# Optimization experiments

Hardware: AMD Instinct MI355X
Metric: run time of the kernel (lower is better)

The kernel has to match this reference:

```python
import jax, jax.numpy as jnp
import numpy as np

N = 200_000      # active voxels
C_IN = 128
C_OUT = 128
GRID = 128
K = 27           # 3x3x3 submanifold kernel offsets
EPS = 1e-4       # scn BatchNormalization default eps
LEAK = 0.333     # scn LeakyReLU default leakiness


def _build_neighbor_idx(rng):
    # unique active voxel coords via unique linear keys in GRID^3
    keys = rng.choice(GRID ** 3, size=N, replace=False).astype(np.int64)
    z = keys % GRID
    y = (keys // GRID) % GRID
    x = keys // (GRID * GRID)
    coords = np.stack([x, y, z], axis=1)  # [N,3]
    order = np.argsort(keys)
    sorted_keys = keys[order]
    offs = np.array([(dx, dy, dz) for dx in (-1, 0, 1)
                     for dy in (-1, 0, 1) for dz in (-1, 0, 1)], dtype=np.int64)
    nb = np.full((N, K), -1, dtype=np.int32)
    for k in range(K):
        q = coords + offs[k]  # [N,3]
        inb = np.all((q >= 0) & (q < GRID), axis=1)
        qk = (q[:, 0] * GRID + q[:, 1]) * GRID + q[:, 2]
        pos = np.searchsorted(sorted_keys, qk)
        pos = np.clip(pos, 0, N - 1)
        hit = inb & (sorted_keys[pos] == qk)
        nb[:, k] = np.where(hit, order[pos].astype(np.int32), -1)
    return nb


def setup_inputs() -> dict:
    key = jax.random.key(0)
    k1, k2 = jax.random.split(key)
    rng = np.random.default_rng(0)
    neighbor_idx = jnp.asarray(_build_neighbor_idx(rng))       # [N,27] int32, -1 = inactive
    features = jax.random.normal(k1, (N, C_IN), dtype=jnp.float32)
    # per-offset conv weights, scn-style init scale
    W = jax.random.normal(k2, (K, C_IN, C_OUT), dtype=jnp.float32) * (1.0 / np.sqrt(K * C_IN))
    b = jnp.zeros((C_OUT,), dtype=jnp.float32)
    gamma = jnp.ones((C_OUT,), dtype=jnp.float32)
    beta = jnp.zeros((C_OUT,), dtype=jnp.float32)
    return {"features": features, "W": W, "b": b, "gamma": gamma,
            "beta": beta, "neighbor_idx": neighbor_idx}


def reference(features, W, b, gamma, beta, neighbor_idx):
    # Submanifold 3D conv: output only at active sites; gather active neighbors.
    valid = (neighbor_idx >= 0)                      # [N,27] bool
    idx = jnp.where(valid, neighbor_idx, 0)          # safe gather index
    out = jnp.broadcast_to(b, (features.shape[0], C_OUT))
    for k in range(K):  # fixed structural loop over 27 kernel offsets
        xk = features[idx[:, k]] * valid[:, k:k + 1].astype(features.dtype)  # [N,C_IN]
        out = out + xk @ W[k]                                                # [N,C_OUT]
    # BatchNormalization over all active sites (training-mode batch stats)
    mean = jnp.mean(out, axis=0)
    var = jnp.var(out, axis=0)
    out = (out - mean) * jax.lax.rsqrt(var + EPS) * gamma + beta
    # LeakyReLU (scn default leakiness 0.333)
    return jnp.where(out > 0, out, LEAK * out)
```

## Files before the change

### kernel.cpp

```cpp
#include <hip/hip_runtime.h>
#include <hip/hip_bf16.h>

#define N_VOX 200000
#define CI 128
#define CO 128
#define KK 27
#define BM 96
#define NBLK96 2084
#define NBLKFB 1563
#define NSTEP 54
#define LEAK 0.333f
#define BN_EPS 1e-4f
#define SENT 0x3FFFFu
#define ACC_STRIDE 132
#define RB_CAP 48
#define RB_PAD 1344

typedef unsigned short u16;
typedef unsigned int u32;
typedef __attribute__((ext_vector_type(8))) short short8;
typedef __attribute__((ext_vector_type(4))) float f32x4;

typedef const __attribute__((address_space(1))) u32* gptr_t;
typedef __attribute__((address_space(3))) u32* lptr_t;

__device__ __forceinline__ u16 f2bf(float f) {
  union { float f; u32 u; } x; x.f = f;
  return (u16)((x.u + 0x7FFFu + ((x.u >> 16) & 1u)) >> 16);
}
__device__ __forceinline__ float bf2f(u16 h) {
  union { u32 u; float f; } x; x.u = ((u32)h) << 16;
  return x.f;
}
__device__ __forceinline__ u16 cvt_bf(float f) {
  union { __hip_bfloat16 h; u16 u; } c;
  c.h = __float2bfloat16(f);
  return c.u;
}
__device__ __forceinline__ int kbase_of(int k) {
  return (k < 13) ? k * RB_CAP : (k == 13 ? 13 * RB_CAP : 13 * RB_CAP + BM + (k - 14) * RB_CAP);
}

__global__ __launch_bounds__(256) void fcast_kernel(const float* __restrict__ f,
                                                    u16* __restrict__ fb) {
  size_t i = ((size_t)blockIdx.x * 256 + threadIdx.x) * 8;
  float4 a = *(const float4*)(f + i);
  float4 b = *(const float4*)(f + i + 4);
  u16 t[8];
  t[0] = cvt_bf(a.x); t[1] = cvt_bf(a.y); t[2] = cvt_bf(a.z); t[3] = cvt_bf(a.w);
  t[4] = cvt_bf(b.x); t[5] = cvt_bf(b.y); t[6] = cvt_bf(b.z); t[7] = cvt_bf(b.w);
  *(uint4*)(fb + i) = *(const uint4*)t;
}

__global__ __launch_bounds__(256) void wcast3_kernel(const float* __restrict__ W,
                                                     u16* __restrict__ Wt3) {
  int gid = blockIdx.x * 256 + threadIdx.x;
  int lane = gid & 63, chunk = gid >> 6;
  int ks = chunk & 3, nf = (chunk >> 2) & 7, k = chunk >> 5;
  int lr = lane & 15, lg = lane >> 4;
  int co = nf * 16 + lr;
  int ci0 = ks * 32 + lg * 8;
  const float* Wk = W + (size_t)k * CI * CO;
  u16 t[8];
#pragma unroll
  for (int e = 0; e < 8; ++e) t[e] = f2bf(Wk[(ci0 + e) * CO + co]);
  *(uint4*)(Wt3 + (size_t)gid * 8) = *(const uint4*)t;
}

__global__ __launch_bounds__(256, 4) void conv_sp_kernel(
    const u16* __restrict__ featb, const u16* __restrict__ Wt3,
    const int* __restrict__ nb, const u16* __restrict__ zp,
    float* __restrict__ out, float* __restrict__ partial) {
  __shared__ __align__(16) char smem[31312];
  u16* const accb = (u16*)smem;
  u32* const rb_lds = (u32*)(smem + 25344);
  int* const cnt_lds = (int*)(smem + 30784);
  int* const wcnt = (int*)(smem + 30896);
  u32* const wl = (u32*)(smem + 30912);
  int* const wl_n = (int*)(smem + 31296);
  float* const ps = (float*)smem;

  const int tid = threadIdx.x;
  const int bid = blockIdx.x;
  const int row0 = bid * BM;
  const int lane = tid & 63;
  const int w = tid >> 6;

  for (int i = tid; i < (BM * ACC_STRIDE) / 2; i += 256) ((u32*)accb)[i] = 0u;
  if (tid < 16) rb_lds[RB_PAD + tid] = SENT;

  {
    const bool inrow = (tid < BM) && (row0 + tid < N_VOX);
    const int* nbp = nb + (size_t)(row0 + tid) * KK;
    int vv[KK];
#pragma unroll
    for (int k = 0; k < KK; ++k) vv[k] = (k != 13 && inrow) ? nbp[k] : -1;
    if (tid < BM)
      rb_lds[13 * RB_CAP + tid] = ((u32)tid << 18) | (inrow ? (u32)(row0 + tid) : SENT);
    if (tid == 0) cnt_lds[13] = BM;
#pragma unroll
    for (int k = 0; k < KK; ++k) {
      if (k == 13) continue;
      bool valid = vv[k] >= 0;
      unsigned long long m = __ballot(valid);
      if (lane == 0) wcnt[w] = (int)__popcll(m);
      __syncthreads();
      int pos = (int)__popcll(m & ((1ull << lane) - 1ull)) + (w == 1 ? wcnt[0] : 0);
      int cnt = wcnt[0] + wcnt[1]; if (cnt > RB_CAP) cnt = RB_CAP;
      int kb = kbase_of(k);
      if (valid && pos < RB_CAP) rb_lds[kb + pos] = ((u32)tid << 18) | (u32)vv[k];
      int pe = (cnt + 15) & ~15;
      for (int i = cnt + tid; i < pe; i += 256) rb_lds[kb + i] = SENT;
      if (tid == 0) cnt_lds[k] = cnt;
      __syncthreads();
    }
  }

  if (tid == 0) {
    int n = 0;
    for (int k = 0; k < KK; ++k) {
      int cnt = cnt_lds[k];
      int kb = kbase_of(k);
      int ntk = (cnt + 15) >> 4;
      for (int t = 0; t < ntk; ++t) wl[n++] = ((u32)k << 11) | (u32)(kb + t * 16);
    }
    if (n & 1) wl[n++] = (u32)RB_PAD;
    wl_n[0] = n;
  }
  __syncthreads();

  const int wv = w;
  const int lr = lane & 15, lg = lane >> 4;
  const int colbase = wv * 32 + lr;
  const int nt = wl_n[0];

  auto loadTile = [&](u32 d, uint4& sc, short8* a) {
    int off = (int)(d & 0x7FFu);
    u32 es = rb_lds[off + lr];
    sc = *(const uint4*)&rb_lds[off + lg * 4];
    u32 src = es & SENT;
    const u16* ap = (src == SENT) ? zp : (featb + (size_t)src * CI);
#pragma unroll
    for (int ks = 0; ks < 4; ++ks) a[ks] = *(const short8*)(ap + ks * 32 + lg * 8);
  };
  auto loadB = [&](u32 d, short8* b) {
    int k = (int)(d >> 11);
    const u16* wb = Wt3 + (size_t)(k * 32 + wv * 8) * 512 + lane * 8;
#pragma unroll
    for (int j = 0; j < 8; ++j) b[j] = *(const short8*)(wb + j * 512);
  };
  auto mfma_scat = [&](const short8* a, const short8* b, const uint4& sc) {
    f32x4 c0 = {0.f, 0.f, 0.f, 0.f}, c1 = {0.f, 0.f, 0.f, 0.f};
#pragma unroll
    for (int ks = 0; ks < 4; ++ks) {
      c0 = __builtin_amdgcn_mfma_f32_16x16x32_bf16(a[ks], b[ks], c0, 0, 0, 0);
      c1 = __builtin_amdgcn_mfma_f32_16x16x32_bf16(a[ks], b[4 + ks], c1, 0, 0, 0);
    }
    u32 e[4] = {sc.x, sc.y, sc.z, sc.w};
#pragma unroll
    for (int r = 0; r < 4; ++r) {
      if (e[r] != SENT) {
        int i0 = (int)(e[r] >> 18) * ACC_STRIDE + colbase;
        accb[i0] = f2bf(bf2f(accb[i0]) + c0[r]);
        accb[i0 + 16] = f2bf(bf2f(accb[i0 + 16]) + c1[r]);
      }
    }
  };

  for (int i = 0; i < nt; i += 2) {
    u32 d0 = wl[i], d1 = wl[i + 1];
    uint4 sc0, sc1;
    short8 a0[4], a1[4], b0[8], b1[8];
    loadTile(d0, sc0, a0);
    loadTile(d1, sc1, a1);
    loadB(d0, b0);
    __builtin_amdgcn_sched_barrier(0);
    mfma_scat(a0, b0, sc0);
    loadB(d1, b1);
    __builtin_amdgcn_sched_barrier(0);
    mfma_scat(a1, b1, sc1);
  }
  __syncthreads();

  float s4[4] = {0.f, 0.f, 0.f, 0.f}, q4[4] = {0.f, 0.f, 0.f, 0.f};
  const int col4 = (tid & 31) * 4;
  const int rgrp = tid >> 5;
#pragma unroll
  for (int i = 0; i < 12; ++i) {
    int row = rgrp + i * 8;
    const u16* ap = &accb[row * ACC_STRIDE + col4];
    float4 v;
    v.x = bf2f(ap[0]); v.y = bf2f(ap[1]); v.z = bf2f(ap[2]); v.w = bf2f(ap[3]);
    int grow = row0 + row;
    if (grow < N_VOX) {
      *(float4*)&out[(size_t)grow * CO + col4] = v;
      s4[0] += v.x; q4[0] += v.x * v.x;
      s4[1] += v.y; q4[1] += v.y * v.y;
      s4[2] += v.z; q4[2] += v.z * v.z;
      s4[3] += v.w; q4[3] += v.w * v.w;
    }
  }
  __syncthreads();
#pragma unroll
  for (int j = 0; j < 4; ++j) {
    ps[rgrp * 128 + col4 + j] = s4[j];
    ps[1024 + rgrp * 128 + col4 + j] = q4[j];
  }
  __syncthreads();
  {
    int col = tid & 127, which = tid >> 7;
    float acc = 0.f;
#pragma unroll
    for (int g = 0; g < 8; ++g) acc += ps[which * 1024 + g * 128 + col];
    partial[(size_t)bid * 256 + tid] = acc;
  }
}

__global__ __launch_bounds__(256, 2) void conv_fb_kernel(
    const float* __restrict__ feat, const u16* __restrict__ Wt3,
    const int* __restrict__ nb, float* __restrict__ out,
    float* __restrict__ partial) {
  __shared__ __align__(16) char smem[46592];
  u16* const Ab = (u16*)smem;
  int* const nbs = (int*)(smem + 32768);
  float* const sq = (float*)smem;

  const int tid = threadIdx.x;
  const int bid = blockIdx.x;
  const int row0 = bid * 128;

  for (int i = tid; i < 128 * KK; i += 256) {
    int gi = row0 * KK + i;
    nbs[i] = (gi < N_VOX * KK) ? nb[gi] : -1;
  }
  __syncthreads();

  const int lane = tid & 63;
  const int wv = tid >> 6;
  const int wr = wv >> 1, wc = wv & 1;
  const int lr = lane & 15, lg = lane >> 4;
  const int arow = tid >> 1;
  const int acol = (tid & 1) * 32;

  f32x4 acc[4][4];
#pragma unroll
  for (int m = 0; m < 4; ++m)
#pragma unroll
    for (int n = 0; n < 4; ++n) acc[m][n] = (f32x4){0.f, 0.f, 0.f, 0.f};

  float4 af[8];
  short8 b0[8], b1[8];

  auto issueAf = [&](int s) {
    int k = s >> 1, half = (s & 1) * 64;
    int src = nbs[arow * KK + k];
    if (src >= 0) {
      const float4* p = (const float4*)(feat + (size_t)src * CI + half + acol);
#pragma unroll
      for (int j = 0; j < 8; ++j) af[j] = p[j];
    } else {
#pragma unroll
      for (int j = 0; j < 8; ++j) af[j] = (float4){0.f, 0.f, 0.f, 0.f};
    }
  };
  auto loadB = [&](int s, short8* bn) {
    int k = s >> 1, half = s & 1;
#pragma unroll
    for (int n = 0; n < 4; ++n)
#pragma unroll
      for (int ks = 0; ks < 2; ++ks)
        bn[n * 2 + ks] = *(const short8*)(Wt3 +
            (size_t)((k * 32 + (wc * 4 + n) * 4) + half * 2 + ks) * 512 + lane * 8);
  };
  auto writeA = [&](u16* Adst) {
    int v = arow & 7;
#pragma unroll
    for (int q = 0; q < 4; ++q) {
      u16 t8[8];
#pragma unroll
      for (int i = 0; i < 2; ++i) {
        float4 f = af[q * 2 + i];
        t8[i * 4 + 0] = cvt_bf(f.x); t8[i * 4 + 1] = cvt_bf(f.y);
        t8[i * 4 + 2] = cvt_bf(f.z); t8[i * 4 + 3] = cvt_bf(f.w);
      }
      int c_o = (tid & 1) * 4 + q;
      *(uint4*)&Adst[arow * 64 + ((c_o ^ v) << 3)] = *(const uint4*)t8;
    }
  };
  auto compute = [&](const u16* A, const short8* bc) {
#pragma unroll
    for (int ks = 0; ks < 2; ++ks) {
      short8 a[4];
#pragma unroll
      for (int m = 0; m < 4; ++m) {
        int r = wr * 64 + m * 16 + lr;
        a[m] = *(const short8*)((const char*)A + r * 128 +
                                ((ks * 64 + lg * 16) ^ ((r & 7) << 4)));
      }
#pragma unroll
      for (int m = 0; m < 4; ++m)
#pragma unroll
        for (int n = 0; n < 4; ++n)
          acc[m][n] = __builtin_amdgcn_mfma_f32_16x16x32_bf16(a[m], bc[n * 2 + ks],
                                                              acc[m][n], 0, 0, 0);
    }
  };

  issueAf(0);
  loadB(0, b0);
  for (int s = 0; s + 2 <= NSTEP - 1; s += 2) {
    writeA(Ab + (s & 1) * 8192); __syncthreads();
    issueAf(s + 1); loadB(s + 1, b1);
    compute(Ab + (s & 1) * 8192, b0);
    writeA(Ab + ((s + 1) & 1) * 8192); __syncthreads();
    issueAf(s + 2); loadB(s + 2, b0);
    compute(Ab + ((s + 1) & 1) * 8192, b1);
  }
  writeA(Ab); __syncthreads();
  issueAf(NSTEP - 1); loadB(NSTEP - 1, b1);
  compute(Ab, b0);
  writeA(Ab + 8192); __syncthreads();
  compute(Ab + 8192, b1);

  float sv[4], qv[4];
#pragma unroll
  for (int n = 0; n < 4; ++n) {
    float s = 0.f, q = 0.f;
    int col = wc * 64 + n * 16 + lr;
#pragma unroll
    for (int m = 0; m < 4; ++m) {
      int rb_ = row0 + wr * 64 + m * 16 + lg * 4;
#pragma unroll
      for (int e = 0; e < 4; ++e) {
        float x = acc[m][n][e];
        if (rb_ + e < N_VOX) out[(size_t)(rb_ + e) * CO + col] = x;
        s += x; q += x * x;
      }
    }
    s += __shfl_xor(s, 16, 64); s += __shfl_xor(s, 32, 64);
    q += __shfl_xor(q, 16, 64); q += __shfl_xor(q, 32, 64);
    sv[n] = s; qv[n] = q;
  }
  __syncthreads();
  if (lg == 0) {
#pragma unroll
    for (int n = 0; n < 4; ++n) {
      int col = wc * 64 + n * 16 + lr;
      sq[wr * 256 + col] = sv[n];
      sq[wr * 256 + 128 + col] = qv[n];
    }
  }
  __syncthreads();
  partial[(size_t)bid * 256 + tid] = sq[tid] + sq[256 + tid];
}

__global__ __launch_bounds__(256) void reduce1_kernel(const float* __restrict__ partial,
                                                      float* __restrict__ partial2,
                                                      int nblk) {
  int t = threadIdx.x, b = blockIdx.x;
  float acc = 0.f;
  int jend = (b + 1) * 16; if (jend > nblk) jend = nblk;
  for (int j = b * 16; j < jend; ++j) acc += partial[(size_t)j * 256 + t];
  partial2[(size_t)b * 256 + t] = acc;
}

__global__ __launch_bounds__(256) void reduce2_kernel(const float* __restrict__ partial2,
                                                      const float* __restrict__ gamma,
                                                      const float* __restrict__ beta,
                                                      float* __restrict__ stats, int n2) {
  __shared__ float sums[256];
  int t = threadIdx.x;
  float acc = 0.f;
  for (int j = 0; j < n2; ++j) acc += partial2[(size_t)j * 256 + t];
  sums[t] = acc;
  __syncthreads();
  if (t < 128) {
    float mean = sums[t] / (float)N_VOX;
    float var = sums[128 + t] / (float)N_VOX - mean * mean;
    float scale = gamma[t] * rsqrtf(var + BN_EPS);
    stats[t] = scale;
    stats[128 + t] = beta[t] - mean * scale;
  }
}

__global__ __launch_bounds__(256) void bnact_kernel(float* __restrict__ out,
                                                    const float* __restrict__ stats) {
  __shared__ float s_scale[128], s_shift[128];
  int t = threadIdx.x;
  if (t < 128) { s_scale[t] = stats[t]; s_shift[t] = stats[128 + t]; }
  __syncthreads();
  size_t i = (size_t)blockIdx.x * 256 + t;
  float4* o4 = (float4*)out;
  float4 v = o4[i];
  int c0 = ((int)(i & 31)) << 2;
  float x;
  x = v.x * s_scale[c0 + 0] + s_shift[c0 + 0]; v.x = x > 0.f ? x : LEAK * x;
  x = v.y * s_scale[c0 + 1] + s_shift[c0 + 1]; v.y = x > 0.f ? x : LEAK * x;
  x = v.z * s_scale[c0 + 2] + s_shift[c0 + 2]; v.z = x > 0.f ? x : LEAK * x;
  x = v.w * s_scale[c0 + 3] + s_shift[c0 + 3]; v.w = x > 0.f ? x : LEAK * x;
  o4[i] = v;
}

extern "C" void kernel_launch(void* const* d_in, const int* in_sizes, int n_in,
                              void* d_out, int out_size, void* d_ws, size_t ws_size,
                              hipStream_t stream) {
  const float* feat  = (const float*)d_in[0];
  const float* W     = (const float*)d_in[1];
  const float* gamma = (const float*)d_in[3];
  const float* beta  = (const float*)d_in[4];
  const int*   nb    = (const int*)d_in[5];
  float* out = (float*)d_out;

  char* ws = (char*)d_ws;
  u16*   Wt3      = (u16*)ws;
  float* partial  = (float*)(ws + 884736);
  float* partial2 = (float*)(ws + 3018752);
  float* stats    = (float*)(ws + 3152896);
  u16*   zp       = (u16*)(ws + 3153920);
  u16*   featb    = (u16*)(ws + 3154176);
  const size_t need_fast = 54354176u;

  hipLaunchKernelGGL(wcast3_kernel, dim3(216), dim3(256), 0, stream, W, Wt3);
  if (ws_size >= need_fast) {
    hipMemsetAsync(zp, 0, 256, stream);
    hipLaunchKernelGGL(fcast_kernel, dim3(12500), dim3(256), 0, stream, feat, featb);
    hipLaunchKernelGGL(conv_sp_kernel, dim3(NBLK96), dim3(256), 0, stream,
                       featb, Wt3, nb, zp, out, partial);
    hipLaunchKernelGGL(reduce1_kernel, dim3(131), dim3(256), 0, stream,
                       partial, partial2, NBLK96);
    hipLaunchKernelGGL(reduce2_kernel, dim3(1), dim3(256), 0, stream,
                       partial2, gamma, beta, stats, 131);
  } else {
    hipLaunchKernelGGL(conv_fb_kernel, dim3(NBLKFB), dim3(256), 0, stream,
                       feat, Wt3, nb, out, partial);
    hipLaunchKernelGGL(reduce1_kernel, dim3(98), dim3(256), 0, stream,
                       partial, partial2, NBLKFB);
    hipLaunchKernelGGL(reduce2_kernel, dim3(1), dim3(256), 0, stream,
                       partial2, gamma, beta, stats, 98);
  }
  hipLaunchKernelGGL(bnact_kernel, dim3(25000), dim3(256), 0, stream, out, stats);
}
```

Baseline: 291.3 us.

## Double rows per block and reuse per-offset weights across tile pairs

Raises the conv block tile from 96 to 192 rows (occupancy bound drops from 4 to 2 blocks per CU) and replaces the flattened worklist with a per-offset loop. Each offset's weight fragments are loaded once and reused over all tiles of that offset, and two tiles are processed together with interleaved MFMAs. This cuts repeated weight loads and halves the number of blocks and partial-stat rows to reduce. The cost is larger LDS use, lower occupancy, and less latency hiding from the removed explicit scheduling barriers.

```diff
diff --git a/kernel.cpp b/kernel.cpp
--- a/kernel.cpp
+++ b/kernel.cpp
@@ -5,16 +5,15 @@
 #define CI 128
 #define CO 128
 #define KK 27
-#define BM 96
-#define NBLK96 2084
+#define BM 192
+#define NBLK192 1042
 #define NBLKFB 1563
 #define NSTEP 54
 #define LEAK 0.333f
 #define BN_EPS 1e-4f
 #define SENT 0x3FFFFu
 #define ACC_STRIDE 132
-#define RB_CAP 48
-#define RB_PAD 1344
+#define RB_CAP 64
 
 typedef unsigned short u16;
 typedef unsigned int u32;
@@ -67,17 +66,15 @@
   *(uint4*)(Wt3 + (size_t)gid * 8) = *(const uint4*)t;
 }
 
-__global__ __launch_bounds__(256, 4) void conv_sp_kernel(
+__global__ __launch_bounds__(256, 2) void conv_sp_kernel(
     const u16* __restrict__ featb, const u16* __restrict__ Wt3,
     const int* __restrict__ nb, const u16* __restrict__ zp,
     float* __restrict__ out, float* __restrict__ partial) {
-  __shared__ __align__(16) char smem[31312];
+  __shared__ __align__(16) char smem[58240];
   u16* const accb = (u16*)smem;
-  u32* const rb_lds = (u32*)(smem + 25344);
-  int* const cnt_lds = (int*)(smem + 30784);
-  int* const wcnt = (int*)(smem + 30896);
-  u32* const wl = (u32*)(smem + 30912);
-  int* const wl_n = (int*)(smem + 31296);
+  u32* const rb_lds = (u32*)(smem + 50688);
+  int* const cnt_lds = (int*)(smem + 58112);
+  int* const wcnt = (int*)(smem + 58224);
   float* const ps = (float*)smem;
 
   const int tid = threadIdx.x;
@@ -87,7 +84,6 @@
   const int w = tid >> 6;
 
   for (int i = tid; i < (BM * ACC_STRIDE) / 2; i += 256) ((u32*)accb)[i] = 0u;
-  if (tid < 16) rb_lds[RB_PAD + tid] = SENT;
 
   {
     const bool inrow = (tid < BM) && (row0 + tid < N_VOX);
@@ -105,8 +101,12 @@
       unsigned long long m = __ballot(valid);
       if (lane == 0) wcnt[w] = (int)__popcll(m);
       __syncthreads();
-      int pos = (int)__popcll(m & ((1ull << lane) - 1ull)) + (w == 1 ? wcnt[0] : 0);
-      int cnt = wcnt[0] + wcnt[1]; if (cnt > RB_CAP) cnt = RB_CAP;
+      int pos = (int)__popcll(m & ((1ull << lane) - 1ull));
+      if (w >= 1) pos += wcnt[0];
+      if (w >= 2) pos += wcnt[1];
+      if (w >= 3) pos += wcnt[2];
+      int cnt = wcnt[0] + wcnt[1] + wcnt[2] + wcnt[3];
+      if (cnt > RB_CAP) cnt = RB_CAP;
       int kb = kbase_of(k);
       if (valid && pos < RB_CAP) rb_lds[kb + pos] = ((u32)tid << 18) | (u32)vv[k];
       int pe = (cnt + 15) & ~15;
@@ -116,26 +116,11 @@
     }
   }
 
-  if (tid == 0) {
-    int n = 0;
-    for (int k = 0; k < KK; ++k) {
-      int cnt = cnt_lds[k];
-      int kb = kbase_of(k);
-      int ntk = (cnt + 15) >> 4;
-      for (int t = 0; t < ntk; ++t) wl[n++] = ((u32)k << 11) | (u32)(kb + t * 16);
-    }
-    if (n & 1) wl[n++] = (u32)RB_PAD;
-    wl_n[0] = n;
-  }
-  __syncthreads();
-
   const int wv = w;
   const int lr = lane & 15, lg = lane >> 4;
   const int colbase = wv * 32 + lr;
-  const int nt = wl_n[0];
-
-  auto loadTile = [&](u32 d, uint4& sc, short8* a) {
-    int off = (int)(d & 0x7FFu);
+
+  auto loadTile = [&](int off, uint4& sc, short8* a) {
     u32 es = rb_lds[off + lr];
     sc = *(const uint4*)&rb_lds[off + lg * 4];
     u32 src = es & SENT;
@@ -143,19 +128,7 @@
 #pragma unroll
     for (int ks = 0; ks < 4; ++ks) a[ks] = *(const short8*)(ap + ks * 32 + lg * 8);
   };
-  auto loadB = [&](u32 d, short8* b) {
-    int k = (int)(d >> 11);
-    const u16* wb = Wt3 + (size_t)(k * 32 + wv * 8) * 512 + lane * 8;
-#pragma unroll
-    for (int j = 0; j < 8; ++j) b[j] = *(const short8*)(wb + j * 512);
-  };
-  auto mfma_scat = [&](const short8* a, const short8* b, const uint4& sc) {
-    f32x4 c0 = {0.f, 0.f, 0.f, 0.f}, c1 = {0.f, 0.f, 0.f, 0.f};
-#pragma unroll
-    for (int ks = 0; ks < 4; ++ks) {
-      c0 = __builtin_amdgcn_mfma_f32_16x16x32_bf16(a[ks], b[ks], c0, 0, 0, 0);
-      c1 = __builtin_amdgcn_mfma_f32_16x16x32_bf16(a[ks], b[4 + ks], c1, 0, 0, 0);
-    }
+  auto scat = [&](const uint4& sc, const f32x4& c0, const f32x4& c1) {
     u32 e[4] = {sc.x, sc.y, sc.z, sc.w};
 #pragma unroll
     for (int r = 0; r < 4; ++r) {
@@ -167,18 +140,47 @@
     }
   };
 
-  for (int i = 0; i < nt; i += 2) {
-    u32 d0 = wl[i], d1 = wl[i + 1];
-    uint4 sc0, sc1;
-    short8 a0[4], a1[4], b0[8], b1[8];
-    loadTile(d0, sc0, a0);
-    loadTile(d1, sc1, a1);
-    loadB(d0, b0);
-    __builtin_amdgcn_sched_barrier(0);
-    mfma_scat(a0, b0, sc0);
-    loadB(d1, b1);
-    __builtin_amdgcn_sched_barrier(0);
-    mfma_scat(a1, b1, sc1);
+  for (int k = 0; k < KK; ++k) {
+    const int cnt = cnt_lds[k];
+    if (cnt == 0) continue;
+    const int ntk = (cnt + 15) >> 4;
+    const int kb = kbase_of(k);
+    short8 b[8];
+    {
+      const u16* wb = Wt3 + (size_t)(k * 32 + wv * 8) * 512 + lane * 8;
+#pragma unroll
+      for (int j = 0; j < 8; ++j) b[j] = *(const short8*)(wb + j * 512);
+    }
+    int t = 0;
+    for (; t + 1 < ntk; t += 2) {
+      uint4 sc0, sc1;
+      short8 a0[4], a1[4];
+      loadTile(kb + t * 16, sc0, a0);
+      loadTile(kb + t * 16 + 16, sc1, a1);
+      f32x4 p0a = {0.f, 0.f, 0.f, 0.f}, p0b = {0.f, 0.f, 0.f, 0.f};
+      f32x4 p1a = {0.f, 0.f, 0.f, 0.f}, p1b = {0.f, 0.f, 0.f, 0.f};
+#pragma unroll
+      for (int ks = 0; ks < 4; ++ks) {
+        p0a = __builtin_amdgcn_mfma_f32_16x16x32_bf16(a0[ks], b[ks], p0a, 0, 0, 0);
+        p1a = __builtin_amdgcn_mfma_f32_16x16x32_bf16(a1[ks], b[ks], p1a, 0, 0, 0);
+        p0b = __builtin_amdgcn_mfma_f32_16x16x32_bf16(a0[ks], b[4 + ks], p0b, 0, 0, 0);
+        p1b = __builtin_amdgcn_mfma_f32_16x16x32_bf16(a1[ks], b[4 + ks], p1b, 0, 0, 0);
+      }
+      scat(sc0, p0a, p0b);
+      scat(sc1, p1a, p1b);
+    }
+    if (t < ntk) {
+      uint4 sc0;
+      short8 a0[4];
+      loadTile(kb + t * 16, sc0, a0);
+      f32x4 p0a = {0.f, 0.f, 0.f, 0.f}, p0b = {0.f, 0.f, 0.f, 0.f};
+#pragma unroll
+      for (int ks = 0; ks < 4; ++ks) {
+        p0a = __builtin_amdgcn_mfma_f32_16x16x32_bf16(a0[ks], b[ks], p0a, 0, 0, 0);
+        p0b = __builtin_amdgcn_mfma_f32_16x16x32_bf16(a0[ks], b[4 + ks], p0b, 0, 0, 0);
+      }
+      scat(sc0, p0a, p0b);
+    }
   }
   __syncthreads();
 
@@ -186,7 +188,7 @@
   const int col4 = (tid & 31) * 4;
   const int rgrp = tid >> 5;
 #pragma unroll
-  for (int i = 0; i < 12; ++i) {
+  for (int i = 0; i < 24; ++i) {
     int row = rgrp + i * 8;
     const u16* ap = &accb[row * ACC_STRIDE + col4];
     float4 v;
@@ -414,22 +416,22 @@
   char* ws = (char*)d_ws;
   u16*   Wt3      = (u16*)ws;
   float* partial  = (float*)(ws + 884736);
-  float* partial2 = (float*)(ws + 3018752);
-  float* stats    = (float*)(ws + 3152896);
-  u16*   zp       = (u16*)(ws + 3153920);
-  u16*   featb    = (u16*)(ws + 3154176);
-  const size_t need_fast = 54354176u;
+  float* partial2 = (float*)(ws + 2485248);
+  float* stats    = (float*)(ws + 2585600);
+  u16*   zp       = (u16*)(ws + 2586624);
+  u16*   featb    = (u16*)(ws + 2586880);
+  const size_t need_fast = 53786880u;
 
   hipLaunchKernelGGL(wcast3_kernel, dim3(216), dim3(256), 0, stream, W, Wt3);
   if (ws_size >= need_fast) {
     hipMemsetAsync(zp, 0, 256, stream);
     hipLaunchKernelGGL(fcast_kernel, dim3(12500), dim3(256), 0, stream, feat, featb);
-    hipLaunchKernelGGL(conv_sp_kernel, dim3(NBLK96), dim3(256), 0, stream,
+    hipLaunchKernelGGL(conv_sp_kernel, dim3(NBLK192), dim3(256), 0, stream,
                        featb, Wt3, nb, zp, out, partial);
-    hipLaunchKernelGGL(reduce1_kernel, dim3(131), dim3(256), 0, stream,
-                       partial, partial2, NBLK96);
+    hipLaunchKernelGGL(reduce1_kernel, dim3(66), dim3(256), 0, stream,
+                       partial, partial2, NBLK192);
     hipLaunchKernelGGL(reduce2_kernel, dim3(1), dim3(256), 0, stream,
-                       partial2, gamma, beta, stats, 131);
+                       partial2, gamma, beta, stats, 66);
   } else {
     hipLaunchKernelGGL(conv_fb_kernel, dim3(NBLKFB), dim3(256), 0, stream,
                        feat, Wt3, nb, out, partial);
```

Measured after the change: 311.5 us. 1.07x slower.

## Software-pipeline gather/weight loads across tiles and remap blocks per XCD

Applied to the files above, without the earlier changes.

Restructures the main tile loop into a double-buffered software pipeline: the A gather and B weight loads for tile i+2 are issued right after the MFMAs for tile i and before its LDS scatter, with s_setprio raised around the MFMAs. It also remaps blockIdx so contiguous row blocks land on the same XCD, aiming for better L2 locality. The odd-count padding entry is dropped and replaced by a tail path. Occupancy drops from 4 to 3 blocks per SM because the extra register buffers raise register pressure.

```diff
diff --git a/kernel.cpp b/kernel.cpp
--- a/kernel.cpp
+++ b/kernel.cpp
@@ -14,7 +14,6 @@
 #define SENT 0x3FFFFu
 #define ACC_STRIDE 132
 #define RB_CAP 48
-#define RB_PAD 1344
 
 typedef unsigned short u16;
 typedef unsigned int u32;
@@ -67,27 +66,28 @@
   *(uint4*)(Wt3 + (size_t)gid * 8) = *(const uint4*)t;
 }
 
-__global__ __launch_bounds__(256, 4) void conv_sp_kernel(
+__global__ __launch_bounds__(256, 3) void conv_sp_kernel(
     const u16* __restrict__ featb, const u16* __restrict__ Wt3,
     const int* __restrict__ nb, const u16* __restrict__ zp,
     float* __restrict__ out, float* __restrict__ partial) {
-  __shared__ __align__(16) char smem[31312];
+  __shared__ __align__(16) char smem[31248];
   u16* const accb = (u16*)smem;
   u32* const rb_lds = (u32*)(smem + 25344);
-  int* const cnt_lds = (int*)(smem + 30784);
-  int* const wcnt = (int*)(smem + 30896);
-  u32* const wl = (u32*)(smem + 30912);
-  int* const wl_n = (int*)(smem + 31296);
+  int* const cnt_lds = (int*)(smem + 30720);
+  int* const wcnt = (int*)(smem + 30832);
+  u32* const wl = (u32*)(smem + 30848);
+  int* const wl_n = (int*)(smem + 31232);
   float* const ps = (float*)smem;
 
   const int tid = threadIdx.x;
-  const int bid = blockIdx.x;
+  const int orig = blockIdx.x;
+  const int xcd = orig & 7, oidx = orig >> 3;
+  const int bid = (xcd < 4) ? xcd * 261 + oidx : 1044 + (xcd - 4) * 260 + oidx;
   const int row0 = bid * BM;
   const int lane = tid & 63;
   const int w = tid >> 6;
 
   for (int i = tid; i < (BM * ACC_STRIDE) / 2; i += 256) ((u32*)accb)[i] = 0u;
-  if (tid < 16) rb_lds[RB_PAD + tid] = SENT;
 
   {
     const bool inrow = (tid < BM) && (row0 + tid < N_VOX);
@@ -124,7 +124,6 @@
       int ntk = (cnt + 15) >> 4;
       for (int t = 0; t < ntk; ++t) wl[n++] = ((u32)k << 11) | (u32)(kb + t * 16);
     }
-    if (n & 1) wl[n++] = (u32)RB_PAD;
     wl_n[0] = n;
   }
   __syncthreads();
@@ -134,28 +133,33 @@
   const int colbase = wv * 32 + lr;
   const int nt = wl_n[0];
 
-  auto loadTile = [&](u32 d, uint4& sc, short8* a) {
+  auto rbRead = [&](u32 d, u32& es, uint4& sc) {
     int off = (int)(d & 0x7FFu);
-    u32 es = rb_lds[off + lr];
+    es = rb_lds[off + lr];
     sc = *(const uint4*)&rb_lds[off + lg * 4];
+  };
+  auto issueA = [&](u32 es, short8* a) {
     u32 src = es & SENT;
     const u16* ap = (src == SENT) ? zp : (featb + (size_t)src * CI);
 #pragma unroll
     for (int ks = 0; ks < 4; ++ks) a[ks] = *(const short8*)(ap + ks * 32 + lg * 8);
   };
-  auto loadB = [&](u32 d, short8* b) {
+  auto issueB = [&](u32 d, short8* b) {
     int k = (int)(d >> 11);
     const u16* wb = Wt3 + (size_t)(k * 32 + wv * 8) * 512 + lane * 8;
 #pragma unroll
     for (int j = 0; j < 8; ++j) b[j] = *(const short8*)(wb + j * 512);
   };
-  auto mfma_scat = [&](const short8* a, const short8* b, const uint4& sc) {
-    f32x4 c0 = {0.f, 0.f, 0.f, 0.f}, c1 = {0.f, 0.f, 0.f, 0.f};
+  auto computeT = [&](const short8* a, const short8* b, f32x4& c0, f32x4& c1) {
+    __builtin_amdgcn_s_setprio(1);
 #pragma unroll
     for (int ks = 0; ks < 4; ++ks) {
       c0 = __builtin_amdgcn_mfma_f32_16x16x32_bf16(a[ks], b[ks], c0, 0, 0, 0);
       c1 = __builtin_amdgcn_mfma_f32_16x16x32_bf16(a[ks], b[4 + ks], c1, 0, 0, 0);
     }
+    __builtin_amdgcn_s_setprio(0);
+  };
+  auto scat4 = [&](const uint4& sc, const f32x4& c0, const f32x4& c1) {
     u32 e[4] = {sc.x, sc.y, sc.z, sc.w};
 #pragma unroll
     for (int r = 0; r < 4; ++r) {
@@ -167,18 +171,40 @@
     }
   };
 
-  for (int i = 0; i < nt; i += 2) {
-    u32 d0 = wl[i], d1 = wl[i + 1];
-    uint4 sc0, sc1;
-    short8 a0[4], a1[4], b0[8], b1[8];
-    loadTile(d0, sc0, a0);
-    loadTile(d1, sc1, a1);
-    loadB(d0, b0);
-    __builtin_amdgcn_sched_barrier(0);
-    mfma_scat(a0, b0, sc0);
-    loadB(d1, b1);
-    __builtin_amdgcn_sched_barrier(0);
-    mfma_scat(a1, b1, sc1);
+  {
+    u32 es0, es1; uint4 sc0, sc1;
+    short8 a0[4], a1[4], b0v[8], b1v[8];
+    u32 d0 = wl[0], d1 = wl[1];
+    rbRead(d0, es0, sc0);
+    rbRead(d1, es1, sc1);
+    issueA(es0, a0); issueB(d0, b0v);
+    issueA(es1, a1); issueB(d1, b1v);
+    int i = 0;
+    for (; i + 1 < nt; i += 2) {
+      {
+        u32 dn = wl[(i + 2 < nt) ? i + 2 : 0];
+        u32 esn; uint4 scn; rbRead(dn, esn, scn);
+        f32x4 c0 = {0.f, 0.f, 0.f, 0.f}, c1 = {0.f, 0.f, 0.f, 0.f};
+        computeT(a0, b0v, c0, c1);
+        issueA(esn, a0); issueB(dn, b0v);
+        scat4(sc0, c0, c1);
+        sc0 = scn;
+      }
+      {
+        u32 dn = wl[(i + 3 < nt) ? i + 3 : 0];
+        u32 esn; uint4 scn; rbRead(dn, esn, scn);
+        f32x4 c0 = {0.f, 0.f, 0.f, 0.f}, c1 = {0.f, 0.f, 0.f, 0.f};
+        computeT(a1, b1v, c0, c1);
+        issueA(esn, a1); issueB(dn, b1v);
+        scat4(sc1, c0, c1);
+        sc1 = scn;
+      }
+    }
+    if (i < nt) {
+      f32x4 c0 = {0.f, 0.f, 0.f, 0.f}, c1 = {0.f, 0.f, 0.f, 0.f};
+      computeT(a0, b0v, c0, c1);
+      scat4(sc0, c0, c1);
+    }
   }
   __syncthreads();
 
```

Result: slower. 298.0 us (+2.3%).
